# Performance work log

Measured on AMD Instinct MI355X. Metric: run time of the kernel, lower is better.

The kernel has to match this reference:

```python
import jax, jax.numpy as jnp
import numpy as np

EMBED = 1280
H = 20
D = 64
MAX_CACHE_LEN = 2048
NEG = -1e30


def setup_inputs() -> dict:
    key = jax.random.key(0)
    ks = jax.random.split(key, 6)
    w = lambda k: jax.random.normal(k, (EMBED, EMBED), dtype=jnp.float32) * 0.02
    return {
        "hidden_states": jax.random.normal(ks[0], (1, 2048, EMBED), dtype=jnp.float32),
        "wq": w(ks[1]), "bq": jnp.zeros((EMBED,), jnp.float32),
        "wk": w(ks[2]),
        "wv": w(ks[3]), "bv": jnp.zeros((EMBED,), jnp.float32),
        "wo": w(ks[4]), "bo": jnp.zeros((EMBED,), jnp.float32),
        "pos_int": 0,
    }


def reference(hidden_states, wq, bq, wk, wv, bv, wo, bo, pos_int):
    B, T, E = hidden_states.shape
    scale = D ** -0.5
    # projections (torch Linear: x @ W^T + b); Whisper k_proj has no bias
    q = (hidden_states @ wq.T + bq).reshape(B, T, H, D).transpose(0, 2, 1, 3)
    k = (hidden_states @ wk.T).reshape(B, T, H, D).transpose(0, 2, 1, 3)
    v = (hidden_states @ wv.T + bv).reshape(B, T, H, D).transpose(0, 2, 1, 3)
    # static KV-cache update (ETKVCache.update): write k,v at [pos:pos+T]
    k_cache = jnp.zeros((B, H, MAX_CACHE_LEN, D), hidden_states.dtype)
    v_cache = jnp.zeros((B, H, MAX_CACHE_LEN, D), hidden_states.dtype)
    k_cache = jax.lax.dynamic_update_slice(k_cache, k, (0, 0, pos_int, 0))
    v_cache = jax.lax.dynamic_update_slice(v_cache, v, (0, 0, pos_int, 0))
    end_pos = pos_int + T
    k_win = k_cache[:, :, :end_pos, :]  # [B,H,S,D]
    v_win = v_cache[:, :, :end_pos, :]
    # SDPA with is_causal=True: torch uses top-left aligned tril(T, S) mask
    scores = jnp.einsum("bhtd,bhsd->bhts", q, k_win) * scale
    mask = jnp.tril(jnp.ones((T, end_pos), dtype=bool))
    scores = jnp.where(mask, scores, NEG)
    attn = jax.nn.softmax(scores, axis=-1)
    out = jnp.einsum("bhts,bhsd->bhtd", attn, v_win)
    out = out.transpose(0, 2, 1, 3).reshape(B, T, H * D)
    return out @ wo.T + bo
```

## Files before the change

kernel.cpp:

```cpp
#include <hip/hip_runtime.h>
#include <hip/hip_bf16.h>

typedef __bf16 bf16;
typedef __bf16 bf16x8 __attribute__((ext_vector_type(8)));
typedef float  f32x4  __attribute__((ext_vector_type(4)));
typedef float  f32x16 __attribute__((ext_vector_type(16)));
typedef unsigned int u32;
typedef u32 u32x4 __attribute__((ext_vector_type(4)));

#define AS1 __attribute__((address_space(1)))
#define AS3 __attribute__((address_space(3)))

#define T_LEN 2048
#define EMB   1280
#define NH    20
#define HD    64

#define QSCALE 0.18033688011112042f

__device__ __forceinline__ void gl_lds16(const void* gsrc, void* ldst) {
  __builtin_amdgcn_global_load_lds((AS1 void*)const_cast<void*>(gsrc),
                                   (AS3 void*)ldst, 16, 0, 0);
}

__global__ __launch_bounds__(256) void cvt_all(
    const float* __restrict__ hs, const float* __restrict__ wq,
    const float* __restrict__ wk, const float* __restrict__ wv,
    const float* __restrict__ wo, bf16* __restrict__ out) {
  const int HS8 = T_LEN * EMB / 8;
  const int W8  = EMB * EMB / 8;
  int i = blockIdx.x * 256 + threadIdx.x;
  const float* src;
  bf16* dst;
  int off;
  if (i < HS8)              { src = hs; dst = out;                              off = i; }
  else if (i < HS8 + W8)    { src = wq; dst = out + (size_t)T_LEN * EMB;        off = i - HS8; }
  else if (i < HS8 + 2*W8)  { src = wk; dst = out + (size_t)T_LEN*EMB +   (size_t)EMB*EMB; off = i - HS8 - W8; }
  else if (i < HS8 + 3*W8)  { src = wv; dst = out + (size_t)T_LEN*EMB + 2*(size_t)EMB*EMB; off = i - HS8 - 2*W8; }
  else if (i < HS8 + 4*W8)  { src = wo; dst = out + (size_t)T_LEN*EMB + 3*(size_t)EMB*EMB; off = i - HS8 - 3*W8; }
  else return;
  const float4* p4 = (const float4*)src;
  float4 a = p4[2 * off], b = p4[2 * off + 1];
  bf16x8 o;
  o[0] = (bf16)a.x; o[1] = (bf16)a.y; o[2] = (bf16)a.z; o[3] = (bf16)a.w;
  o[4] = (bf16)b.x; o[5] = (bf16)b.y; o[6] = (bf16)b.z; o[7] = (bf16)b.w;
  *(bf16x8*)(dst + (size_t)off * 8) = o;
}

template<int MT>
__global__ __launch_bounds__(256, 2) void gemm_nt(
    const bf16* __restrict__ hsb, const bf16* __restrict__ aob,
    const bf16* __restrict__ wqb, const bf16* __restrict__ wkb,
    const bf16* __restrict__ wvb, const bf16* __restrict__ wob,
    const float* __restrict__ bq, const float* __restrict__ bv,
    const float* __restrict__ bo,
    bf16* __restrict__ Qb, bf16* __restrict__ Kb, bf16* __restrict__ VTb,
    float* __restrict__ Out, int kind)
{
  constexpr int BM = MT * 32;
  __shared__ alignas(16) bf16 As[BM * 64];
  __shared__ alignas(16) bf16 Bs[128 * 64];

  const int mode = (kind == 0) ? (int)blockIdx.y : 3;
  const bf16* A = (kind == 0) ? hsb : aob;
  const bf16* B = (mode == 0) ? wqb : (mode == 1) ? wkb : (mode == 2) ? wvb : wob;

  const int bm = blockIdx.x / 10;
  const int bn = blockIdx.x % 10;
  const int lane = threadIdx.x & 63;
  const int w = threadIdx.x >> 6;
  const int wr = w >> 1, wc = w & 1;
  const int g = lane >> 4, c = lane & 15;

  const f32x4 z4 = {0.f, 0.f, 0.f, 0.f};
  f32x4 acc[MT][4];
  #pragma unroll
  for (int i = 0; i < MT; ++i)
    #pragma unroll
    for (int j = 0; j < 4; ++j) acc[i][j] = z4;

  for (int kt = 0; kt < EMB / 64; ++kt) {
    #pragma unroll
    for (int i = 0; i < MT; ++i) {
      const int call = w * MT + i;
      const int slot = call * 1024 + lane * 16;
      const int row = slot >> 7;
      const int scb = (slot & 127) ^ ((row & 7) << 4);
      gl_lds16((const char*)A + (size_t)(bm * BM + row) * (EMB * 2) + kt * 128 + scb,
               (char*)As + call * 1024);
    }
    #pragma unroll
    for (int i = 0; i < 4; ++i) {
      const int call = w * 4 + i;
      const int slot = call * 1024 + lane * 16;
      const int row = slot >> 7;
      const int scb = (slot & 127) ^ ((row & 7) << 4);
      gl_lds16((const char*)B + (size_t)(bn * 128 + row) * (EMB * 2) + kt * 128 + scb,
               (char*)Bs + call * 1024);
    }
    __syncthreads();
    #pragma unroll
    for (int kc = 0; kc < 2; ++kc) {
      bf16x8 af[MT], bfr[4];
      #pragma unroll
      for (int mt = 0; mt < MT; ++mt) {
        const int row = wr * (MT * 16) + mt * 16 + c;
        const int off = row * 128 + ((kc * 64 + g * 16) ^ ((row & 7) << 4));
        af[mt] = *(const bf16x8*)((const char*)As + off);
      }
      #pragma unroll
      for (int nt = 0; nt < 4; ++nt) {
        const int row = wc * 64 + nt * 16 + c;
        const int off = row * 128 + ((kc * 64 + g * 16) ^ ((row & 7) << 4));
        bfr[nt] = *(const bf16x8*)((const char*)Bs + off);
      }
      #pragma unroll
      for (int mt = 0; mt < MT; ++mt)
        #pragma unroll
        for (int nt = 0; nt < 4; ++nt)
          acc[mt][nt] = __builtin_amdgcn_mfma_f32_16x16x32_bf16(af[mt], bfr[nt],
                                                                acc[mt][nt], 0, 0, 0);
    }
    __syncthreads();
  }

  #pragma unroll
  for (int mt = 0; mt < MT; ++mt) {
    const int t0 = bm * BM + wr * (MT * 16) + mt * 16 + g * 4;
    #pragma unroll
    for (int nt = 0; nt < 4; ++nt) {
      const int n = bn * 128 + wc * 64 + nt * 16 + c;
      const int h = n >> 6, d = n & 63;
      #pragma unroll
      for (int r = 0; r < 4; ++r) {
        const int t = t0 + r;
        float v = acc[mt][nt][r];
        if (mode == 0) {
          v = (v + bq[n]) * QSCALE;
          Qb[((size_t)h * T_LEN + t) * HD + d] = (bf16)v;
        } else if (mode == 1) {
          Kb[((size_t)h * T_LEN + t) * HD + d] = (bf16)v;
        } else if (mode == 2) {
          v += bv[n];
          VTb[((size_t)h * HD + d) * T_LEN + t] = (bf16)v;
        } else {
          Out[(size_t)t * EMB + n] = v + bo[n];
        }
      }
    }
  }
}

__global__ __launch_bounds__(256, 2) void attn_fwd(
    const bf16* __restrict__ Qb, const bf16* __restrict__ Kb,
    const bf16* __restrict__ VTb, bf16* __restrict__ AOb)
{
  __shared__ alignas(16) bf16 kbuf[2][64 * 64];
  __shared__ alignas(16) bf16 vbuf[2][64 * 64];

  const int bid = blockIdx.x;
  const int h  = bid % NH;
  const int qb = (T_LEN / 128 - 1) - bid / NH;
  const int lane = threadIdx.x & 63;
  const int w  = threadIdx.x >> 6;
  const int l31 = lane & 31;
  const int hi  = lane >> 5;
  const int q0 = qb * 128;
  const int qw = q0 + w * 32;
  const int q  = qw + l31;

  bf16x8 qf[4];
  {
    const char* qrow = (const char*)Qb + ((size_t)h * T_LEN + q) * (HD * 2);
    #pragma unroll
    for (int ds = 0; ds < 4; ++ds)
      qf[ds] = *(const bf16x8*)(qrow + ds * 32 + hi * 16);
  }

  f32x16 oacc[2];
  #pragma unroll
  for (int r = 0; r < 16; ++r) { oacc[0][r] = 0.f; oacc[1][r] = 0.f; }
  float m_r = -1e30f, ls = 0.f;

  auto STAGE = [&](int b, int j) {
    const int s0 = j * 64;
    #pragma unroll
    for (int i = 0; i < 2; ++i) {
      const int call = w * 2 + i;
      const int slot = call * 1024 + lane * 16;
      const int row = slot >> 7;
      const int col = (slot & 127) ^ ((row & 7) << 4);
      gl_lds16((const char*)Kb + ((size_t)h * T_LEN + s0 + row) * (HD * 2) + col,
               (char*)kbuf[b] + call * 1024);
      gl_lds16((const char*)VTb + (((size_t)h * HD + row) * T_LEN + s0) * 2 + col,
               (char*)vbuf[b] + call * 1024);
    }
  };

  auto AFRAG = [&](const bf16* buf, int rblk, int colb) -> bf16x8 {
    const int row = rblk * 32 + l31;
    const int off = row * 128 + ((colb + hi * 16) ^ ((row & 7) << 4));
    return *(const bf16x8*)((const char*)buf + off);
  };

  STAGE(0, 0);
  int cur = 0;
  const int nj = 2 * qb + 2;
  for (int j = 0; j < nj; ++j) {
    STAGE(cur ^ 1, j + 1 < nj ? j + 1 : j);
    asm volatile("s_waitcnt vmcnt(4)" ::: "memory");
    __builtin_amdgcn_s_barrier();
    asm volatile("" ::: "memory");

    f32x16 sv[2];
    #pragma unroll
    for (int r = 0; r < 16; ++r) { sv[0][r] = 0.f; sv[1][r] = 0.f; }
    #pragma unroll
    for (int ds = 0; ds < 4; ++ds) {
      #pragma unroll
      for (int sb = 0; sb < 2; ++sb) {
        bf16x8 kf = AFRAG(kbuf[cur], sb, ds * 32);
        sv[sb] = __builtin_amdgcn_mfma_f32_32x32x16_bf16(kf, qf[ds], sv[sb], 0, 0, 0);
      }
    }

    if (j >= 2 * qb) {
      const int s0 = j * 64;
      #pragma unroll
      for (int sb = 0; sb < 2; ++sb)
        #pragma unroll
        for (int r = 0; r < 16; ++r) {
          const int s = s0 + sb * 32 + (r & 3) + 8 * (r >> 2) + 4 * hi;
          if (s > q) sv[sb][r] = -1e30f;
        }
    }

    float pm = sv[0][0];
    #pragma unroll
    for (int r = 1; r < 16; ++r) pm = fmaxf(pm, sv[0][r]);
    #pragma unroll
    for (int r = 0; r < 16; ++r) pm = fmaxf(pm, sv[1][r]);
    pm = fmaxf(pm, __shfl_xor(pm, 32));
    const float mn = fmaxf(m_r, pm);
    const float sc = __builtin_amdgcn_exp2f(m_r - mn);
    m_r = mn;
    float ps = 0.f;
    #pragma unroll
    for (int sb = 0; sb < 2; ++sb)
      #pragma unroll
      for (int r = 0; r < 16; ++r) {
        const float p = __builtin_amdgcn_exp2f(sv[sb][r] - mn);
        sv[sb][r] = p;
        ps += p;
      }
    ls = ls * sc + ps;
    oacc[0] *= sc;
    oacc[1] *= sc;

    u32 wds[16], xds[16];
    #pragma unroll
    for (int i = 0; i < 8; ++i) {
      asm("v_cvt_pk_bf16_f32 %0, %1, %2" : "=v"(wds[i])     : "v"(sv[0][2*i]), "v"(sv[0][2*i+1]));
      asm("v_cvt_pk_bf16_f32 %0, %1, %2" : "=v"(wds[8 + i]) : "v"(sv[1][2*i]), "v"(sv[1][2*i+1]));
    }
    #pragma unroll
    for (int i = 0; i < 16; ++i) xds[i] = (u32)__shfl_xor((int)wds[i], 32);

    #pragma unroll
    for (int ks = 0; ks < 4; ++ks) {
      const int o = (ks >> 1) * 8 + (ks & 1) * 4;
      u32x4 fw;
      fw.x = hi ? xds[o + 2] : wds[o];
      fw.y = hi ? xds[o + 3] : wds[o + 1];
      fw.z = hi ? wds[o + 2] : xds[o];
      fw.w = hi ? wds[o + 3] : xds[o + 1];
      bf16x8 pf = __builtin_bit_cast(bf16x8, fw);
      #pragma unroll
      for (int db = 0; db < 2; ++db) {
        bf16x8 vf = AFRAG(vbuf[cur], db, ks * 32);
        oacc[db] = __builtin_amdgcn_mfma_f32_32x32x16_bf16(vf, pf, oacc[db], 0, 0, 0);
      }
    }

    asm volatile("" ::: "memory");
    __builtin_amdgcn_s_barrier();
    cur ^= 1;
  }

  const float lt = ls + __shfl_xor(ls, 32);
  const float inv = 1.f / lt;
  char* orow = (char*)AOb + ((size_t)q * EMB + h * HD) * 2;
  #pragma unroll
  for (int db = 0; db < 2; ++db)
    #pragma unroll
    for (int i = 0; i < 8; ++i) {
      const float lo = oacc[db][2 * i] * inv;
      const float hv = oacc[db][2 * i + 1] * inv;
      u32 pk;
      asm("v_cvt_pk_bf16_f32 %0, %1, %2" : "=v"(pk) : "v"(lo), "v"(hv));
      const int d = db * 32 + ((2 * i) & 3) + 8 * (i >> 1) + 4 * hi;
      *(u32*)(orow + d * 2) = pk;
    }
}

extern "C" void kernel_launch(void* const* d_in, const int* in_sizes, int n_in,
                              void* d_out, int out_size, void* d_ws, size_t ws_size,
                              hipStream_t stream) {
  const float* hs = (const float*)d_in[0];
  const float* wq = (const float*)d_in[1];
  const float* bq = (const float*)d_in[2];
  const float* wk = (const float*)d_in[3];
  const float* wv = (const float*)d_in[4];
  const float* bv = (const float*)d_in[5];
  const float* wo = (const float*)d_in[6];
  const float* bo = (const float*)d_in[7];

  bf16* p = (bf16*)d_ws;
  bf16* hsb = p;  p += (size_t)T_LEN * EMB;
  bf16* wqb = p;  p += (size_t)EMB * EMB;
  bf16* wkb = p;  p += (size_t)EMB * EMB;
  bf16* wvb = p;  p += (size_t)EMB * EMB;
  bf16* wob = p;  p += (size_t)EMB * EMB;
  bf16* Qb  = p;  p += (size_t)NH * T_LEN * HD;
  bf16* Kb  = p;  p += (size_t)NH * T_LEN * HD;
  bf16* VTb = p;  p += (size_t)NH * HD * T_LEN;
  bf16* AOb = p;  p += (size_t)T_LEN * EMB;

  const int TOT8 = T_LEN * EMB / 8 + 4 * (EMB * EMB / 8);
  cvt_all<<<(TOT8 + 255) / 256, 256, 0, stream>>>(hs, wq, wk, wv, wo, (bf16*)d_ws);

  gemm_nt<4><<<dim3(160, 3), 256, 0, stream>>>(hsb, AOb, wqb, wkb, wvb, wob, bq, bv, bo,
                                               Qb, Kb, VTb, (float*)d_out, 0);
  attn_fwd<<<dim3(320), 256, 0, stream>>>(Qb, Kb, VTb, AOb);
  gemm_nt<2><<<dim3(320, 1), 256, 0, stream>>>(hsb, AOb, wqb, wkb, wvb, wob, bq, bv, bo,
                                               Qb, Kb, VTb, (float*)d_out, 1);
}
```

Measured before the change: 122.6 us.

## Split causal attention across KV chunks with combine pass; double-buffer GEMM loads

```diff
diff --git a/kernel.cpp b/kernel.cpp
--- a/kernel.cpp
+++ b/kernel.cpp
@@ -15,6 +15,8 @@
 #define EMB   1280
 #define NH    20
 #define HD    64
+
+#define NCHUNK_PER_HEAD 40
 
 #define QSCALE 0.18033688011112042f
 
@@ -58,8 +60,9 @@
     float* __restrict__ Out, int kind)
 {
   constexpr int BM = MT * 32;
-  __shared__ alignas(16) bf16 As[BM * 64];
-  __shared__ alignas(16) bf16 Bs[128 * 64];
+  constexpr int NK = EMB / 64;
+  __shared__ alignas(16) bf16 As[2][BM * 64];
+  __shared__ alignas(16) bf16 Bs[2][128 * 64];
 
   const int mode = (kind == 0) ? (int)blockIdx.y : 3;
   const bf16* A = (kind == 0) ? hsb : aob;
@@ -79,7 +82,7 @@
     #pragma unroll
     for (int j = 0; j < 4; ++j) acc[i][j] = z4;
 
-  for (int kt = 0; kt < EMB / 64; ++kt) {
+  auto STAGE = [&](int b, int kt) {
     #pragma unroll
     for (int i = 0; i < MT; ++i) {
       const int call = w * MT + i;
@@ -87,7 +90,7 @@
       const int row = slot >> 7;
       const int scb = (slot & 127) ^ ((row & 7) << 4);
       gl_lds16((const char*)A + (size_t)(bm * BM + row) * (EMB * 2) + kt * 128 + scb,
-               (char*)As + call * 1024);
+               (char*)As[b] + call * 1024);
     }
     #pragma unroll
     for (int i = 0; i < 4; ++i) {
@@ -96,9 +99,20 @@
       const int row = slot >> 7;
       const int scb = (slot & 127) ^ ((row & 7) << 4);
       gl_lds16((const char*)B + (size_t)(bn * 128 + row) * (EMB * 2) + kt * 128 + scb,
-               (char*)Bs + call * 1024);
-    }
-    __syncthreads();
+               (char*)Bs[b] + call * 1024);
+    }
+  };
+
+  STAGE(0, 0);
+  for (int kt = 0; kt < NK; ++kt) {
+    const int cur = kt & 1;
+    STAGE(cur ^ 1, kt + 1 < NK ? kt + 1 : kt);
+    if constexpr (MT == 4) asm volatile("s_waitcnt vmcnt(8)" ::: "memory");
+    else                   asm volatile("s_waitcnt vmcnt(6)" ::: "memory");
+    __builtin_amdgcn_s_barrier();
+    asm volatile("" ::: "memory");
+    const bf16* Asc = As[cur];
+    const bf16* Bsc = Bs[cur];
     #pragma unroll
     for (int kc = 0; kc < 2; ++kc) {
       bf16x8 af[MT], bfr[4];
@@ -106,13 +120,13 @@
       for (int mt = 0; mt < MT; ++mt) {
         const int row = wr * (MT * 16) + mt * 16 + c;
         const int off = row * 128 + ((kc * 64 + g * 16) ^ ((row & 7) << 4));
-        af[mt] = *(const bf16x8*)((const char*)As + off);
+        af[mt] = *(const bf16x8*)((const char*)Asc + off);
       }
       #pragma unroll
       for (int nt = 0; nt < 4; ++nt) {
         const int row = wc * 64 + nt * 16 + c;
         const int off = row * 128 + ((kc * 64 + g * 16) ^ ((row & 7) << 4));
-        bfr[nt] = *(const bf16x8*)((const char*)Bs + off);
+        bfr[nt] = *(const bf16x8*)((const char*)Bsc + off);
       }
       #pragma unroll
       for (int mt = 0; mt < MT; ++mt)
@@ -121,7 +135,8 @@
           acc[mt][nt] = __builtin_amdgcn_mfma_f32_16x16x32_bf16(af[mt], bfr[nt],
                                                                 acc[mt][nt], 0, 0, 0);
     }
-    __syncthreads();
+    asm volatile("" ::: "memory");
+    __builtin_amdgcn_s_barrier();
   }
 
   #pragma unroll
@@ -151,23 +166,32 @@
   }
 }
 
-__global__ __launch_bounds__(256, 2) void attn_fwd(
+__global__ __launch_bounds__(256, 4) void attn_fwd(
     const bf16* __restrict__ Qb, const bf16* __restrict__ Kb,
-    const bf16* __restrict__ VTb, bf16* __restrict__ AOb)
+    const bf16* __restrict__ VTb, bf16* __restrict__ AOb,
+    bf16* __restrict__ Pob, float* __restrict__ Pml)
 {
   __shared__ alignas(16) bf16 kbuf[2][64 * 64];
   __shared__ alignas(16) bf16 vbuf[2][64 * 64];
 
   const int bid = blockIdx.x;
-  const int h  = bid % NH;
-  const int qb = (T_LEN / 128 - 1) - bid / NH;
+  const int h   = bid / NCHUNK_PER_HEAD;
+  const int idx = (NCHUNK_PER_HEAD - 1) - bid % NCHUNK_PER_HEAD;
+  int qb, ch, nch;
+  if (idx < 4)       { qb = idx;                ch = 0;      nch = 1; }
+  else if (idx < 12) { int t = idx - 4;  qb = 4 + (t >> 1);  ch = t & 1;  nch = 2; }
+  else if (idx < 24) { int t = idx - 12; qb = 8 + t / 3;     ch = t % 3;  nch = 3; }
+  else               { int t = idx - 24; qb = 12 + (t >> 2); ch = t & 3;  nch = 4; }
+  const int nj = 2 * qb + 2;
+  const int j0 = ch * 8;
+  const int j1 = (j0 + 8 < nj) ? j0 + 8 : nj;
+
   const int lane = threadIdx.x & 63;
   const int w  = threadIdx.x >> 6;
   const int l31 = lane & 31;
   const int hi  = lane >> 5;
   const int q0 = qb * 128;
-  const int qw = q0 + w * 32;
-  const int q  = qw + l31;
+  const int q  = q0 + w * 32 + l31;
 
   bf16x8 qf[4];
   {
@@ -203,11 +227,10 @@
     return *(const bf16x8*)((const char*)buf + off);
   };
 
-  STAGE(0, 0);
+  STAGE(0, j0);
   int cur = 0;
-  const int nj = 2 * qb + 2;
-  for (int j = 0; j < nj; ++j) {
-    STAGE(cur ^ 1, j + 1 < nj ? j + 1 : j);
+  for (int j = j0; j < j1; ++j) {
+    STAGE(cur ^ 1, j + 1 < j1 ? j + 1 : j);
     asm volatile("s_waitcnt vmcnt(4)" ::: "memory");
     __builtin_amdgcn_s_barrier();
     asm volatile("" ::: "memory");
@@ -288,19 +311,75 @@
   }
 
   const float lt = ls + __shfl_xor(ls, 32);
-  const float inv = 1.f / lt;
-  char* orow = (char*)AOb + ((size_t)q * EMB + h * HD) * 2;
-  #pragma unroll
-  for (int db = 0; db < 2; ++db)
-    #pragma unroll
-    for (int i = 0; i < 8; ++i) {
-      const float lo = oacc[db][2 * i] * inv;
-      const float hv = oacc[db][2 * i + 1] * inv;
-      u32 pk;
-      asm("v_cvt_pk_bf16_f32 %0, %1, %2" : "=v"(pk) : "v"(lo), "v"(hv));
-      const int d = db * 32 + ((2 * i) & 3) + 8 * (i >> 1) + 4 * hi;
-      *(u32*)(orow + d * 2) = pk;
-    }
+
+  if (nch == 1) {
+    const float inv = 1.f / lt;
+    char* orow = (char*)AOb + ((size_t)q * EMB + h * HD) * 2;
+    #pragma unroll
+    for (int db = 0; db < 2; ++db)
+      #pragma unroll
+      for (int i = 0; i < 8; ++i) {
+        const float lo = oacc[db][2 * i] * inv;
+        const float hv = oacc[db][2 * i + 1] * inv;
+        u32 pk;
+        asm("v_cvt_pk_bf16_f32 %0, %1, %2" : "=v"(pk) : "v"(lo), "v"(hv));
+        const int d = db * 32 + 8 * (i >> 1) + 2 * (i & 1) + 4 * hi;
+        *(u32*)(orow + d * 2) = pk;
+      }
+  } else {
+    const int pi = h * NCHUNK_PER_HEAD + idx;
+    const int rowloc = w * 32 + l31;
+    bf16* pr = Pob + ((size_t)pi * 128 + rowloc) * 64;
+    #pragma unroll
+    for (int db = 0; db < 2; ++db)
+      #pragma unroll
+      for (int i = 0; i < 8; ++i) {
+        u32 pk;
+        asm("v_cvt_pk_bf16_f32 %0, %1, %2" : "=v"(pk) : "v"(oacc[db][2*i]), "v"(oacc[db][2*i+1]));
+        const int d = db * 32 + 8 * (i >> 1) + 2 * (i & 1) + 4 * hi;
+        *(u32*)((char*)pr + d * 2) = pk;
+      }
+    if (hi == 0) {
+      float* ml = Pml + ((size_t)pi * 128 + rowloc) * 2;
+      ml[0] = m_r;
+      ml[1] = lt;
+    }
+  }
+}
+
+__global__ __launch_bounds__(256) void attn_combine(
+    const bf16* __restrict__ Pob, const float* __restrict__ Pml,
+    bf16* __restrict__ AOb)
+{
+  const int gw = (blockIdx.x * 256 + threadIdx.x) >> 6;
+  const int lane = threadIdx.x & 63;
+  const int h  = gw / 1536;
+  const int rr = gw % 1536;
+  const int qb = 4 + rr / 128;
+  const int rl = rr % 128;
+  const int nch   = (qb < 8) ? 2 : (qb < 12) ? 3 : 4;
+  const int ibase = (qb < 8) ? 4 + 2 * (qb - 4)
+                   : (qb < 12) ? 12 + 3 * (qb - 8)
+                   : 24 + 4 * (qb - 12);
+  const int pi0 = h * NCHUNK_PER_HEAD + ibase;
+
+  float mv[4], lv[4];
+  float m = -1e30f;
+  for (int c2 = 0; c2 < nch; ++c2) {
+    const float* ml = Pml + ((size_t)(pi0 + c2) * 128 + rl) * 2;
+    mv[c2] = ml[0];
+    lv[c2] = ml[1];
+    m = fmaxf(m, mv[c2]);
+  }
+  float acc = 0.f, l = 0.f;
+  for (int c2 = 0; c2 < nch; ++c2) {
+    const float sc = __builtin_amdgcn_exp2f(mv[c2] - m);
+    const float ov = (float)Pob[((size_t)(pi0 + c2) * 128 + rl) * 64 + lane];
+    acc += sc * ov;
+    l   += sc * lv[c2];
+  }
+  const int qrow = qb * 128 + rl;
+  AOb[(size_t)qrow * EMB + h * HD + lane] = (bf16)(acc / l);
 }
 
 extern "C" void kernel_launch(void* const* d_in, const int* in_sizes, int n_in,
@@ -326,12 +405,16 @@
   bf16* VTb = p;  p += (size_t)NH * HD * T_LEN;
   bf16* AOb = p;  p += (size_t)T_LEN * EMB;
 
+  bf16*  Pob = (bf16*)d_ws;
+  float* Pml = (float*)((char*)d_ws + (size_t)NH * NCHUNK_PER_HEAD * 128 * 64 * 2);
+
   const int TOT8 = T_LEN * EMB / 8 + 4 * (EMB * EMB / 8);
   cvt_all<<<(TOT8 + 255) / 256, 256, 0, stream>>>(hs, wq, wk, wv, wo, (bf16*)d_ws);
 
   gemm_nt<4><<<dim3(160, 3), 256, 0, stream>>>(hsb, AOb, wqb, wkb, wvb, wob, bq, bv, bo,
                                                Qb, Kb, VTb, (float*)d_out, 0);
-  attn_fwd<<<dim3(320), 256, 0, stream>>>(Qb, Kb, VTb, AOb);
+  attn_fwd<<<dim3(NH * NCHUNK_PER_HEAD), 256, 0, stream>>>(Qb, Kb, VTb, AOb, Pob, Pml);
+  attn_combine<<<dim3(NH * 1536 / 4), 256, 0, stream>>>(Pob, Pml, AOb);
   gemm_nt<2><<<dim3(320, 1), 256, 0, stream>>>(hsb, AOb, wqb, wkb, wvb, wob, bq, bv, bo,
                                                Qb, Kb, VTb, (float*)d_out, 1);
 }
```

Result: faster. 119.5 us (-2.6%).
